# Kernel optimization log

Measured on AMD Instinct MI355X. Metric: run time of the kernel, lower is better.

The kernel has to match this reference:

```python
import jax, jax.numpy as jnp
import numpy as np

B, S, D = 4, 2048, 2048          # batch, seq_len, num_hiddens (= query/key/value size)
H = 16                           # num_heads
DH = D // H                      # head dim = shared K/V projection dim


def setup_inputs() -> dict:
    key = jax.random.key(0)
    ks = jax.random.split(key, 11)
    s_in = 1.0 / np.sqrt(D)
    return {
        "q": jax.random.normal(ks[0], (B, S, D), jnp.float32),
        "k": jax.random.normal(ks[1], (B, S, D), jnp.float32),
        "v": jax.random.normal(ks[2], (B, S, D), jnp.float32),
        "Wq": jax.random.normal(ks[3], (D, D), jnp.float32) * s_in,
        "bq": jnp.zeros((D,), jnp.float32),
        "Wk": jax.random.normal(ks[4], (D, DH), jnp.float32) * s_in,
        "bk": jnp.zeros((DH,), jnp.float32),
        "Wv": jax.random.normal(ks[5], (D, DH), jnp.float32) * s_in,
        "bv": jnp.zeros((DH,), jnp.float32),
        "Wo": jax.random.normal(ks[6], (D, D), jnp.float32) * s_in,
        "bo": jnp.zeros((D,), jnp.float32),
    }


def reference(q, k, v, Wq, bq, Wk, bk, Wv, bv, Wo, bo):
    # Projections
    qh = (q @ Wq + bq).reshape(B, S, H, DH).transpose(0, 2, 1, 3)  # [B,H,S,DH]
    kh = k @ Wk + bk                                               # [B,S,DH] shared K head
    vh = v @ Wv + bv                                               # [B,S,DH] shared V head
    # Scaled dot-product attention with broadcast-shared K/V (no copies)
    scores = jnp.einsum('bhqd,bkd->bhqk', qh, kh) / jnp.sqrt(jnp.float32(DH))
    attn = jax.nn.softmax(scores, axis=-1)                          # [B,H,S,S]
    out = jnp.einsum('bhqk,bkd->bhqd', attn, vh)                    # [B,H,S,DH]
    out = out.transpose(0, 2, 1, 3).reshape(B, S, D)                # merge heads
    return out @ Wo + bo
```

## Files before the change

kernel.cpp:

```cpp
#include <hip/hip_runtime.h>
#include <stdint.h>

#define B_  4
#define S_  2048
#define D_  2048
#define H_  16
#define DH_ 128
#define M_  (B_*S_)

typedef unsigned short u16;
typedef __bf16 bf16x8 __attribute__((ext_vector_type(8)));
typedef float  f32x4  __attribute__((ext_vector_type(4)));
typedef u16    u16x4  __attribute__((ext_vector_type(4)));

__device__ __forceinline__ u16 f2bf(float f){
  unsigned x = __float_as_uint(f);
  x += 0x7fffu + ((x >> 16) & 1u);
  return (u16)(x >> 16);
}

__device__ __forceinline__ unsigned pkbf(float lo, float hi){
  unsigned r;
  asm("v_cvt_pk_bf16_f32 %0, %1, %2" : "=v"(r) : "v"(lo), "v"(hi));
  return r;
}

__device__ __forceinline__ void stage16(const void* g, void* lds_base){
  __builtin_amdgcn_global_load_lds(
      (const __attribute__((address_space(1))) void*)g,
      (__attribute__((address_space(3))) void*)lds_base, 16, 0, 0);
}

__device__ __forceinline__ f32x4 mfma16(bf16x8 a, bf16x8 b, f32x4 c){
  return __builtin_amdgcn_mfma_f32_16x16x32_bf16(a, b, c, 0, 0, 0);
}

__global__ void cvt_bf16(const float* __restrict__ s, u16* __restrict__ d, int n4){
  int i = blockIdx.x * 256 + threadIdx.x;
  if (i >= n4) return;
  float4 f = ((const float4*)s)[i];
  u16x4 u = { f2bf(f.x), f2bf(f.y), f2bf(f.z), f2bf(f.w) };
  ((u16x4*)d)[i] = u;
}

__global__ void cvt_bf16_2(const float* __restrict__ s0, const float* __restrict__ s1,
                           u16* __restrict__ d0, u16* __restrict__ d1, int n4){
  const float* s = blockIdx.y ? s1 : s0;
  u16*        d = blockIdx.y ? d1 : d0;
  int i = blockIdx.x * 256 + threadIdx.x;
  if (i >= n4) return;
  float4 f = ((const float4*)s)[i];
  u16x4 u = { f2bf(f.x), f2bf(f.y), f2bf(f.z), f2bf(f.w) };
  ((u16x4*)d)[i] = u;
}

__global__ void transpose_bf(const float* __restrict__ W, u16* __restrict__ WT, int K, int N){
  __shared__ float tl[32][33];
  int n0 = blockIdx.x * 32, k0 = blockIdx.y * 32;
  int tx = threadIdx.x, ty = threadIdx.y;
  for (int r = 0; r < 4; r++)
    tl[ty + 8*r][tx] = W[(size_t)(k0 + ty + 8*r) * N + n0 + tx];
  __syncthreads();
  for (int r = 0; r < 4; r++)
    WT[(size_t)(n0 + ty + 8*r) * K + k0 + tx] = f2bf(tl[tx][ty + 8*r]);
}

__global__ void transpose_vh(const u16* __restrict__ vh, u16* __restrict__ vhT){
  __shared__ u16 tl[32][33];
  int b = blockIdx.z, d0 = blockIdx.x * 32, s0 = blockIdx.y * 32;
  int tx = threadIdx.x, ty = threadIdx.y;
  for (int r = 0; r < 4; r++)
    tl[ty + 8*r][tx] = vh[(size_t)(b * S_ + s0 + ty + 8*r) * DH_ + d0 + tx];
  __syncthreads();
  for (int r = 0; r < 4; r++)
    vhT[(size_t)(b * DH_ + d0 + ty + 8*r) * S_ + s0 + tx] = tl[tx][ty + 8*r];
}

template<int OUTF32>
__global__ __launch_bounds__(256) void gemm_bt(const u16* __restrict__ A,
    const u16* __restrict__ BT, const float* __restrict__ bias, void* __restrict__ Cv,
    int M, int N, int K)
{
  (void)M;
  __shared__ alignas(16) u16 Al[128 * 32];
  __shared__ alignas(16) u16 Bl[128 * 32];
  const int t = threadIdx.x, lane = t & 63, wave = t >> 6;
  const int quad = lane >> 4, lcol = lane & 15;
  const int m0 = blockIdx.y * 128, n0 = blockIdx.x * 128;
  const int wm = (wave >> 1) * 64, wn = (wave & 1) * 64;
  f32x4 acc[4][4] = {};
  for (int k0 = 0; k0 < K; k0 += 32) {
    for (int p = 0; p < 2; p++) {
      int c = p * 256 + wave * 64 + lane;
      int row = c >> 2, kc = c & 3;
      stage16(A  + (size_t)(m0 + row) * K + k0 + kc * 8, Al + (p*256 + wave*64) * 8);
      stage16(BT + (size_t)(n0 + row) * K + k0 + kc * 8, Bl + (p*256 + wave*64) * 8);
    }
    __syncthreads();
    bf16x8 af[4], bfr[4];
    for (int i = 0; i < 4; i++)
      af[i]  = *(const bf16x8*)(Al + (wm + i*16 + lcol) * 32 + quad * 8);
    for (int j = 0; j < 4; j++)
      bfr[j] = *(const bf16x8*)(Bl + (wn + j*16 + lcol) * 32 + quad * 8);
    for (int i = 0; i < 4; i++)
      for (int j = 0; j < 4; j++)
        acc[i][j] = mfma16(af[i], bfr[j], acc[i][j]);
    __syncthreads();
  }
  for (int j = 0; j < 4; j++) {
    int n = n0 + wn + j * 16 + lcol;
    float bj = bias[n];
    for (int i = 0; i < 4; i++) {
      int mbase = m0 + wm + i * 16 + quad * 4;
      for (int r = 0; r < 4; r++) {
        float vv = acc[i][j][r] + bj;
        if (OUTF32) ((float*)Cv)[(size_t)(mbase + r) * N + n] = vv;
        else        ((u16*)Cv)  [(size_t)(mbase + r) * N + n] = f2bf(vv);
      }
    }
  }
}

__global__ __launch_bounds__(256) void gemm_kv(
    const u16* __restrict__ A0, const u16* __restrict__ A1,
    const u16* __restrict__ BT0, const u16* __restrict__ BT1,
    const float* __restrict__ b0, const float* __restrict__ b1,
    u16* __restrict__ C0, u16* __restrict__ C1)
{
  const int sel = blockIdx.z;
  const u16* A  = sel ? A1 : A0;
  const u16* BT = sel ? BT1 : BT0;
  const float* bias = sel ? b1 : b0;
  u16* C = sel ? C1 : C0;

  __shared__ alignas(16) u16 Al[32 * 32];
  __shared__ alignas(16) u16 Bl[128 * 32];
  const int t = threadIdx.x, lane = t & 63, wave = t >> 6;
  const int quad = lane >> 4, lcol = lane & 15;
  const int m0 = blockIdx.x * 32;

  f32x4 acc[2][2] = {};
  for (int k0 = 0; k0 < D_; k0 += 32) {
    if (t < 128) {
      int row = t >> 2, kc = t & 3;
      stage16(A + (size_t)(m0 + row) * D_ + k0 + kc * 8, Al + (wave * 64) * 8);
    } else {
      int bc = t - 128, row = bc >> 2, kc = bc & 3;
      stage16(BT + (size_t)row * D_ + k0 + kc * 8, Bl + ((wave - 2) * 64) * 8);
    }
    {
      int bc = t + 128, row = bc >> 2, kc = bc & 3;
      stage16(BT + (size_t)row * D_ + k0 + kc * 8, Bl + (128 + wave * 64) * 8);
    }
    if (t < 128) {
      int bc = t + 384, row = bc >> 2, kc = bc & 3;
      stage16(BT + (size_t)row * D_ + k0 + kc * 8, Bl + (384 + wave * 64) * 8);
    }
    __syncthreads();
    bf16x8 af[2], bfr[2];
    for (int i = 0; i < 2; i++)
      af[i]  = *(const bf16x8*)(Al + (i*16 + lcol) * 32 + quad * 8);
    for (int j = 0; j < 2; j++)
      bfr[j] = *(const bf16x8*)(Bl + (wave*32 + j*16 + lcol) * 32 + quad * 8);
    for (int i = 0; i < 2; i++)
      for (int j = 0; j < 2; j++)
        acc[i][j] = mfma16(af[i], bfr[j], acc[i][j]);
    __syncthreads();
  }
  for (int j = 0; j < 2; j++) {
    int n = wave * 32 + j * 16 + lcol;
    float bj = bias[n];
    for (int i = 0; i < 2; i++) {
      int mbase = m0 + i * 16 + quad * 4;
      for (int r = 0; r < 4; r++)
        C[(size_t)(mbase + r) * DH_ + n] = f2bf(acc[i][j][r] + bj);
    }
  }
}

__global__ __launch_bounds__(256, 3) void mqa_attn(const u16* __restrict__ qh,
    const u16* __restrict__ kh, const u16* __restrict__ vhT, u16* __restrict__ ao)
{
  __shared__ alignas(16) u16 Kl[2][32 * 128];
  __shared__ alignas(16) u16 Vl[2][128 * 32];
  const int t = threadIdx.x, lane = t & 63, wave = t >> 6;
  const int quad = lane >> 4, lcol = lane & 15;
  const int b = blockIdx.z, h = blockIdx.y;
  const int q0 = blockIdx.x * 128 + wave * 32;
  const float sc2 = 0.12751743f;

  bf16x8 qf[2][4];
  for (int m = 0; m < 2; m++) {
    const u16* qp = qh + (size_t)(b * S_ + q0 + m * 16 + lcol) * D_ + h * DH_ + quad * 8;
    for (int kk = 0; kk < 4; kk++) qf[m][kk] = *(const bf16x8*)(qp + kk * 32);
  }
  union { u16 u[8]; bf16x8 v; } one_u;
  for (int i = 0; i < 8; i++) one_u.u[i] = 0x3F80;
  const bf16x8 ones = one_u.v;

  f32x4 o[2][8] = {};
  f32x4 al[2] = {};
  const u16* kb = kh  + (size_t)b * S_ * DH_;
  const u16* vb = vhT + (size_t)b * DH_ * S_;

  auto stageKV = [&](int tt, int bi) {
    int kv0 = tt * 32;
    for (int p = 0; p < 2; p++) {
      int c = p * 256 + wave * 64 + lane;
      int row = c >> 4, st = c & 15;
      int kc = st ^ (row & 15);
      stage16(kb + (size_t)(kv0 + row) * DH_ + kc * 8, &Kl[bi][(p*256 + wave*64) * 8]);
    }
    for (int p = 0; p < 2; p++) {
      int c = p * 256 + wave * 64 + lane;
      int row = c >> 2, st = c & 3;
      int kc = st ^ (row & 3) ^ ((row >> 2) & 3);
      stage16(vb + (size_t)row * S_ + kv0 + kc * 8, &Vl[bi][(p*256 + wave*64) * 8]);
    }
  };

  stageKV(0, 0);
  for (int tt = 0; tt < S_ / 32; tt++) {
    const int bi = tt & 1;
    __syncthreads();
    if (tt < S_ / 32 - 1) stageKV(tt + 1, bi ^ 1);

    const u16* Kb = &Kl[bi][0];
    const u16* Vb = &Vl[bi][0];

    unsigned cc[2][4];
    for (int kvf = 0; kvf < 2; kvf++) {
      f32x4 s[2] = {};
      const u16* kp = Kb + (size_t)(kvf * 16 + lcol) * 128;
      __builtin_amdgcn_s_setprio(1);
      for (int kk = 0; kk < 4; kk++) {
        int swz = (kk * 4 + quad) ^ lcol;
        bf16x8 kfr = *(const bf16x8*)(kp + swz * 8);
        for (int m = 0; m < 2; m++)
          s[m] = mfma16(kfr, qf[m][kk], s[m]);
      }
      __builtin_amdgcn_s_setprio(0);
      for (int m = 0; m < 2; m++) {
        float e0 = exp2f(s[m][0] * sc2), e1 = exp2f(s[m][1] * sc2);
        float e2 = exp2f(s[m][2] * sc2), e3 = exp2f(s[m][3] * sc2);
        cc[m][kvf * 2 + 0] = pkbf(e0, e1);
        cc[m][kvf * 2 + 1] = pkbf(e2, e3);
      }
    }
    bf16x8 pa[2];
    for (int m = 0; m < 2; m++) {
      asm("v_permlane32_swap_b32 %0, %1" : "+v"(cc[m][0]), "+v"(cc[m][2]));
      asm("v_permlane16_swap_b32 %0, %1" : "+v"(cc[m][0]), "+v"(cc[m][2]));
      asm("v_permlane32_swap_b32 %0, %1" : "+v"(cc[m][1]), "+v"(cc[m][3]));
      asm("v_permlane16_swap_b32 %0, %1" : "+v"(cc[m][1]), "+v"(cc[m][3]));
      union { unsigned u[4]; bf16x8 v; } pu;
      pu.u[0] = cc[m][0];
      pu.u[1] = cc[m][1];
      pu.u[2] = cc[m][2];
      pu.u[3] = cc[m][3];
      pa[m] = pu.v;
    }

    __builtin_amdgcn_s_setprio(1);
    for (int g = 0; g < 8; g++) {
      int swz = quad ^ (lcol & 3) ^ ((lcol >> 2) & 3);
      bf16x8 vfr = *(const bf16x8*)(Vb + (size_t)(g * 16 + lcol) * 32 + swz * 8);
      for (int m = 0; m < 2; m++)
        o[m][g] = mfma16(pa[m], vfr, o[m][g]);
    }
    for (int m = 0; m < 2; m++)
      al[m] = mfma16(pa[m], ones, al[m]);
    __builtin_amdgcn_s_setprio(0);
  }

  for (int m = 0; m < 2; m++) {
    u16* op = ao + (size_t)(b * S_ + q0 + m * 16 + quad * 4) * D_ + h * DH_ + lcol;
    for (int r = 0; r < 4; r++) {
      float inv = 1.0f / al[m][r];
      for (int g = 0; g < 8; g++)
        op[(size_t)r * D_ + g * 16] = f2bf(o[m][g][r] * inv);
    }
  }
}

extern "C" void kernel_launch(void* const* d_in, const int* in_sizes, int n_in,
                              void* d_out, int out_size, void* d_ws, size_t ws_size,
                              hipStream_t stream)
{
  (void)in_sizes; (void)n_in; (void)out_size;
  const float* q  = (const float*)d_in[0];
  const float* k  = (const float*)d_in[1];
  const float* v  = (const float*)d_in[2];
  const float* Wq = (const float*)d_in[3];
  const float* bq = (const float*)d_in[4];
  const float* Wk = (const float*)d_in[5];
  const float* bk = (const float*)d_in[6];
  const float* Wv = (const float*)d_in[7];
  const float* bv = (const float*)d_in[8];
  const float* Wo = (const float*)d_in[9];
  const float* bo = (const float*)d_in[10];
  float* out = (float*)d_out;

  char* ws = (char*)d_ws;
  size_t off = 0;
  auto alloc = [&](size_t bytes) -> char* {
    char* p = ws + off; off += (bytes + 255) & ~(size_t)255; return p;
  };
  u16* xbf = (u16*)alloc((size_t)M_ * D_ * 2);
  u16* qh  = (u16*)alloc((size_t)M_ * D_ * 2);
  u16* kh  = (u16*)alloc((size_t)M_ * DH_ * 2);
  u16* vh  = (u16*)alloc((size_t)M_ * DH_ * 2);
  u16* vhT = (u16*)alloc((size_t)M_ * DH_ * 2);
  u16* WqT = (u16*)alloc((size_t)D_ * D_ * 2);
  u16* WkT = (u16*)alloc((size_t)DH_ * D_ * 2);
  u16* WvT = (u16*)alloc((size_t)DH_ * D_ * 2);
  u16* WoT = (u16*)alloc((size_t)D_ * D_ * 2);
  u16* ao  = xbf;

  if (off > ws_size) return;

  const int n4 = M_ * D_ / 4;

  transpose_bf<<<dim3(D_/32,  D_/32), dim3(32, 8), 0, stream>>>(Wq, WqT, D_, D_);
  transpose_bf<<<dim3(DH_/32, D_/32), dim3(32, 8), 0, stream>>>(Wk, WkT, D_, DH_);
  transpose_bf<<<dim3(DH_/32, D_/32), dim3(32, 8), 0, stream>>>(Wv, WvT, D_, DH_);
  transpose_bf<<<dim3(D_/32,  D_/32), dim3(32, 8), 0, stream>>>(Wo, WoT, D_, D_);

  cvt_bf16_2<<<dim3(n4 / 256, 2), dim3(256), 0, stream>>>(k, v, xbf, qh, n4);
  gemm_kv<<<dim3(M_/32, 1, 2), dim3(256), 0, stream>>>(
      xbf, qh, WkT, WvT, bk, bv, kh, vh);
  transpose_vh<<<dim3(DH_/32, S_/32, B_), dim3(32, 8), 0, stream>>>(vh, vhT);
  cvt_bf16<<<dim3(n4 / 256), dim3(256), 0, stream>>>(q, xbf, n4);
  gemm_bt<0><<<dim3(D_/128,  M_/128), dim3(256), 0, stream>>>(xbf, WqT, bq, qh, M_, D_, D_);

  mqa_attn<<<dim3(S_/128, H_, B_), dim3(256), 0, stream>>>(qh, kh, vhT, ao);

  gemm_bt<1><<<dim3(D_/128, M_/128), dim3(256), 0, stream>>>(ao, WoT, bo, out, M_, D_, D_);
}
```

Measured before the change: 684.5 us.

## Replace 128x128 GEMM with 256x256 double-buffered swizzled 8-wave pipelined GEMM

Replaces the simple 128x128-tile bf16 GEMM used for the Q and output projections with a 256x256-tile, 512-thread kernel. It uses XOR-swizzled LDS, double-buffered 64-wide K slabs, and interleaves the next tile's global loads across four quadrant MFMA phases with explicit waitcnt, barriers and setprio. The aim is to raise arithmetic intensity per byte loaded, hide global memory latency and avoid LDS bank conflicts. In exchange it hardcodes the 2048 dimensions and relies on delicate manual synchronisation, and with one block per CU plus larger tiles, occupancy and tile-count balance on the CUs may suffer.

```diff
diff --git a/kernel.cpp b/kernel.cpp
--- a/kernel.cpp
+++ b/kernel.cpp
@@ -77,45 +77,100 @@
 }
 
 template<int OUTF32>
-__global__ __launch_bounds__(256) void gemm_bt(const u16* __restrict__ A,
-    const u16* __restrict__ BT, const float* __restrict__ bias, void* __restrict__ Cv,
-    int M, int N, int K)
+__global__ __launch_bounds__(512, 1) void gemm256(const u16* __restrict__ A,
+    const u16* __restrict__ BT, const float* __restrict__ bias, void* __restrict__ Cv)
 {
-  (void)M;
-  __shared__ alignas(16) u16 Al[128 * 32];
-  __shared__ alignas(16) u16 Bl[128 * 32];
+  __shared__ alignas(16) u16 AB[2][2][2 * 128 * 64];
   const int t = threadIdx.x, lane = t & 63, wave = t >> 6;
   const int quad = lane >> 4, lcol = lane & 15;
-  const int m0 = blockIdx.y * 128, n0 = blockIdx.x * 128;
-  const int wm = (wave >> 1) * 64, wn = (wave & 1) * 64;
-  f32x4 acc[4][4] = {};
-  for (int k0 = 0; k0 < K; k0 += 32) {
-    for (int p = 0; p < 2; p++) {
-      int c = p * 256 + wave * 64 + lane;
-      int row = c >> 2, kc = c & 3;
-      stage16(A  + (size_t)(m0 + row) * K + k0 + kc * 8, Al + (p*256 + wave*64) * 8);
-      stage16(BT + (size_t)(n0 + row) * K + k0 + kc * 8, Bl + (p*256 + wave*64) * 8);
-    }
-    __syncthreads();
-    bf16x8 af[4], bfr[4];
-    for (int i = 0; i < 4; i++)
-      af[i]  = *(const bf16x8*)(Al + (wm + i*16 + lcol) * 32 + quad * 8);
-    for (int j = 0; j < 4; j++)
-      bfr[j] = *(const bf16x8*)(Bl + (wn + j*16 + lcol) * 32 + quad * 8);
-    for (int i = 0; i < 4; i++)
-      for (int j = 0; j < 4; j++)
-        acc[i][j] = mfma16(af[i], bfr[j], acc[i][j]);
-    __syncthreads();
-  }
-  for (int j = 0; j < 4; j++) {
-    int n = n0 + wn + j * 16 + lcol;
-    float bj = bias[n];
-    for (int i = 0; i < 4; i++) {
-      int mbase = m0 + wm + i * 16 + quad * 4;
-      for (int r = 0; r < 4; r++) {
-        float vv = acc[i][j][r] + bj;
-        if (OUTF32) ((float*)Cv)[(size_t)(mbase + r) * N + n] = vv;
-        else        ((u16*)Cv)  [(size_t)(mbase + r) * N + n] = f2bf(vv);
+  const int wr = wave >> 1, wc = wave & 1;
+  const int m0 = blockIdx.y * 256, n0 = blockIdx.x * 256;
+  const int NT = 2048 / 64;
+
+  auto stageH = [&](const u16* g, int grow0, int kcol0, u16* lb){
+    #pragma unroll
+    for (int i = 0; i < 2; i++){
+      int l = (i*8 + wave)*64 + lane;
+      int row = l >> 3, st = l & 7;
+      int c = st ^ (row & 7);
+      stage16(g + (size_t)(grow0 + row)*2048 + kcol0 + c*8, lb + (size_t)(i*8 + wave)*512);
+    }
+  };
+
+  f32x4 acc[4][2][4] = {};
+
+  stageH(A,  m0,       0,  &AB[0][0][0]);
+  stageH(BT, n0,       0,  &AB[0][1][0]);
+  stageH(BT, n0 + 128, 0,  &AB[0][1][8192]);
+  stageH(A,  m0 + 128, 0,  &AB[0][0][8192]);
+  stageH(A,  m0,       64, &AB[1][0][0]);
+  stageH(BT, n0 + 128, 64, &AB[1][1][8192]);
+  asm volatile("s_waitcnt vmcnt(4)" ::: "memory");
+  __builtin_amdgcn_s_barrier();
+
+  for (int T = 0; T < NT; ++T) {
+    const int bi = T & 1;
+    const u16* Ab = &AB[bi][0][0];
+    const u16* Bb = &AB[bi][1][0];
+    #pragma unroll
+    for (int q = 0; q < 4; ++q) {
+      const int ah = q >> 1, bh = (q >> 1) ^ (q & 1);
+      bf16x8 af[2][2], bv[4][2];
+      #pragma unroll
+      for (int m = 0; m < 2; m++) {
+        const u16* ap = Ab + (size_t)(ah*128 + wr*32 + m*16 + lcol) * 64;
+        #pragma unroll
+        for (int kk = 0; kk < 2; kk++)
+          af[m][kk] = *(const bf16x8*)(ap + (((kk*4 + quad) ^ (lcol & 7)) * 8));
+      }
+      #pragma unroll
+      for (int n = 0; n < 4; n++) {
+        const u16* bp = Bb + (size_t)(bh*128 + wc*64 + n*16 + lcol) * 64;
+        #pragma unroll
+        for (int kk = 0; kk < 2; kk++)
+          bv[n][kk] = *(const bf16x8*)(bp + (((kk*4 + quad) ^ (lcol & 7)) * 8));
+      }
+      if      (q == 0 && T + 1 < NT) stageH(BT, n0,       (T+1)*64, &AB[(T+1)&1][1][0]);
+      else if (q == 1 && T + 1 < NT) stageH(A,  m0 + 128, (T+1)*64, &AB[(T+1)&1][0][8192]);
+      else if (q == 2 && T + 2 < NT) stageH(A,  m0,       (T+2)*64, &AB[bi][0][0]);
+      else if (q == 3 && T + 2 < NT) stageH(BT, n0 + 128, (T+2)*64, &AB[bi][1][8192]);
+
+      __builtin_amdgcn_s_barrier();
+      asm volatile("s_waitcnt lgkmcnt(0)" ::: "memory");
+      __builtin_amdgcn_sched_barrier(0);
+      __builtin_amdgcn_s_setprio(1);
+      #pragma unroll
+      for (int m = 0; m < 2; m++)
+        #pragma unroll
+        for (int n = 0; n < 4; n++)
+          #pragma unroll
+          for (int kk = 0; kk < 2; kk++)
+            acc[q][m][n] = mfma16(af[m][kk], bv[n][kk], acc[q][m][n]);
+      __builtin_amdgcn_s_setprio(0);
+      if (q == 3) {
+        if (T < NT - 2) { asm volatile("s_waitcnt vmcnt(4)" ::: "memory"); }
+        else            { asm volatile("s_waitcnt vmcnt(0)" ::: "memory"); }
+      }
+      __builtin_amdgcn_s_barrier();
+    }
+  }
+
+  #pragma unroll
+  for (int q = 0; q < 4; ++q) {
+    const int ah = q >> 1, bh = (q >> 1) ^ (q & 1);
+    #pragma unroll
+    for (int n = 0; n < 4; n++) {
+      int col = n0 + bh*128 + wc*64 + n*16 + lcol;
+      float bj = bias[col];
+      #pragma unroll
+      for (int m = 0; m < 2; m++) {
+        int rowb = m0 + ah*128 + wr*32 + m*16 + quad*4;
+        #pragma unroll
+        for (int r = 0; r < 4; r++) {
+          float vv = acc[q][m][n][r] + bj;
+          if (OUTF32) ((float*)Cv)[(size_t)(rowb + r) * 2048 + col] = vv;
+          else        ((u16*)Cv)  [(size_t)(rowb + r) * 2048 + col] = f2bf(vv);
+        }
       }
     }
   }
@@ -331,9 +386,9 @@
       xbf, qh, WkT, WvT, bk, bv, kh, vh);
   transpose_vh<<<dim3(DH_/32, S_/32, B_), dim3(32, 8), 0, stream>>>(vh, vhT);
   cvt_bf16<<<dim3(n4 / 256), dim3(256), 0, stream>>>(q, xbf, n4);
-  gemm_bt<0><<<dim3(D_/128,  M_/128), dim3(256), 0, stream>>>(xbf, WqT, bq, qh, M_, D_, D_);
+  gemm256<0><<<dim3(D_/256, M_/256), dim3(512), 0, stream>>>(xbf, WqT, bq, qh);
 
   mqa_attn<<<dim3(S_/128, H_, B_), dim3(256), 0, stream>>>(qh, kh, vhT, ao);
 
-  gemm_bt<1><<<dim3(D_/128, M_/128), dim3(256), 0, stream>>>(ao, WoT, bo, out, M_, D_, D_);
-}
+  gemm256<1><<<dim3(D_/256, M_/256), dim3(512), 0, stream>>>(ao, WoT, bo, out);
+}
```

New measurement: 613.5 us. 10.4% less time.
